# Kernel tuning notes

Measured on AMD Instinct MI355X. Metric: run time of the kernel, lower is better.

Reference implementation:

```python
import jax, jax.numpy as jnp
import numpy as np
from functools import partial

VS, VT, E, H = 32000, 32000, 512, 1024
B, S, T = 32, 64, 64


def gru_cell(x, h, Wih, Whh, bih, bhh):
    # PyTorch GRU gate order: r, z, n
    gi = x @ Wih.T + bih
    gh = h @ Whh.T + bhh
    ir, iz, inn = jnp.split(gi, 3, axis=-1)
    hr, hz, hn = jnp.split(gh, 3, axis=-1)
    r = jax.nn.sigmoid(ir + hr)
    z = jax.nn.sigmoid(iz + hz)
    n = jnp.tanh(inn + r * hn)
    return (1.0 - z) * n + z * h


def setup_inputs() -> dict:
    key = jax.random.key(0)
    ks = jax.random.split(key, 20)
    s = 0.02
    src = jax.random.randint(ks[0], (B, S), 0, VS)
    tgt = jax.random.randint(ks[1], (B, T), 0, VT)
    src_embed = (jax.random.normal(ks[2], (VS, E)) * s).at[0].set(0.0)  # padding_idx=0
    tgt_embed = (jax.random.normal(ks[3], (VT, E)) * s).at[0].set(0.0)
    enc_Wih = jax.random.normal(ks[4], (3 * H, E)) * s
    enc_Whh = jax.random.normal(ks[5], (3 * H, H)) * s
    enc_bih = jax.random.normal(ks[6], (3 * H,)) * s
    enc_bhh = jax.random.normal(ks[7], (3 * H,)) * s
    dec_Wih = jax.random.normal(ks[8], (3 * H, E + H)) * s
    dec_Whh = jax.random.normal(ks[9], (3 * H, H)) * s
    dec_bih = jax.random.normal(ks[10], (3 * H,)) * s
    dec_bhh = jax.random.normal(ks[11], (3 * H,)) * s
    attn_W = jax.random.normal(ks[12], (E, 2 * H)) * s
    attn_b = jax.random.normal(ks[13], (E,)) * s
    v_w = jax.random.normal(ks[14], (E,)) * s
    fc_W = jax.random.normal(ks[15], (VT, H)) * s
    fc_b = jax.random.normal(ks[16], (VT,)) * s
    return dict(src=src, tgt=tgt, src_embed=src_embed, tgt_embed=tgt_embed,
                enc_Wih=enc_Wih, enc_Whh=enc_Whh, enc_bih=enc_bih, enc_bhh=enc_bhh,
                dec_Wih=dec_Wih, dec_Whh=dec_Whh, dec_bih=dec_bih, dec_bhh=dec_bhh,
                attn_W=attn_W, attn_b=attn_b, v_w=v_w, fc_W=fc_W, fc_b=fc_b)


def reference(src, tgt, src_embed, tgt_embed, enc_Wih, enc_Whh, enc_bih, enc_bhh,
              dec_Wih, dec_Whh, dec_bih, dec_bhh, attn_W, attn_b, v_w, fc_W, fc_b):
    # --- encoder: GRU over src ---
    src_emb = src_embed[src]                      # [B,S,E]
    h0 = jnp.zeros((src.shape[0], H), src_emb.dtype)

    def enc_step(h, x):
        h2 = gru_cell(x, h, enc_Wih, enc_Whh, enc_bih, enc_bhh)
        return h2, h2

    h_last, enc_seq = jax.lax.scan(enc_step, h0, jnp.swapaxes(src_emb, 0, 1))
    enc = jnp.swapaxes(enc_seq, 0, 1)             # [B,S,H] encoder_outputs

    # attn linear splits: cat([hidden, enc]) @ attn_W.T == h@Wh.T + enc@We.T
    Wh, We = attn_W[:, :H], attn_W[:, H:]
    enc_proj = jnp.einsum('bsh,eh->bse', enc, We) + attn_b  # [B,S,E]

    # --- decoder with teacher forcing ratio = 1.0 (deterministic) ---
    def dec_step(h, tok):
        emb = tgt_embed[tok]                              # [B,E]
        energy = jnp.tanh(enc_proj + (h @ Wh.T)[:, None, :])  # [B,S,E]
        scores = jnp.einsum('bse,e->bs', energy, v_w)
        w = jax.nn.softmax(scores, axis=1)                # [B,S]
        ctx = jnp.einsum('bs,bsh->bh', w, enc)            # [B,H]
        x = jnp.concatenate([emb, ctx], axis=-1)          # [B,E+H]
        h2 = gru_cell(x, h, dec_Wih, dec_Whh, dec_bih, dec_bhh)
        logits = h2 @ fc_W.T + fc_b                       # [B,VT]
        return h2, logits

    _, logits = jax.lax.scan(dec_step, h_last, tgt[:, :-1].T)  # [T-1,B,VT]
    return jnp.swapaxes(logits, 0, 1)                     # [B,T-1,VT]
```

## Files before the change

kernel.cpp:

```cpp
#include <hip/hip_runtime.h>
#include <hip/hip_bf16.h>

typedef __hip_bfloat16 bf16;
typedef __attribute__((ext_vector_type(8))) __bf16 bf16x8;
typedef __attribute__((ext_vector_type(4))) float f32x4;
typedef __attribute__((ext_vector_type(4))) unsigned int u32x4;

#define DEVI __device__ __forceinline__

DEVI float sigm(float x) { return 1.f / (1.f + __expf(-x)); }
DEVI float tanh_fast(float x) { float e = __expf(2.f * x); return 1.f - 2.f / (e + 1.f); }
DEVI float lo2f(unsigned u) { return __uint_as_float(u << 16); }
DEVI float hi2f(unsigned u) { return __uint_as_float(u & 0xffff0000u); }

DEVI __bf16 f2b(float f) {
    unsigned u = __float_as_uint(f);
    u = u + 0x7FFFu + ((u >> 16) & 1u);
    unsigned short s = (unsigned short)(u >> 16);
    __bf16 b;
    __builtin_memcpy(&b, &s, 2);
    return b;
}
DEVI unsigned short b2u(__bf16 b) { unsigned short s; __builtin_memcpy(&s, &b, 2); return s; }

DEVI f32x4 MFMA(bf16x8 a, bf16x8 b, f32x4 c) {
    return __builtin_amdgcn_mfma_f32_16x16x32_bf16(a, b, c, 0, 0, 0);
}

DEVI bf16x8 load8(const bf16* p) { return *reinterpret_cast<const bf16x8*>(p); }
DEVI bf16x8 load8(const float* p) {
    float4 a = *reinterpret_cast<const float4*>(p);
    float4 b = *reinterpret_cast<const float4*>(p + 4);
    bf16x8 r;
    r[0] = f2b(a.x); r[1] = f2b(a.y); r[2] = f2b(a.z); r[3] = f2b(a.w);
    r[4] = f2b(b.x); r[5] = f2b(b.y); r[6] = f2b(b.z); r[7] = f2b(b.w);
    return r;
}

DEVI void storeOut(float* p, float v) { *p = v; }
DEVI void storeOut(bf16* p, float v) { *p = __float2bfloat16(v); }

#define WAIT_COHERENT() do { \
    asm volatile("s_waitcnt vmcnt(0)" ::: "memory"); \
    __builtin_amdgcn_sched_barrier(0); } while (0)

DEVI bf16x8 ld_cv16(const bf16* p) {
    u32x4 r;
    asm volatile("global_load_dwordx4 %0, %1, off sc0 sc1"
                 : "=v"(r) : "v"(p) : "memory");
    bf16x8 out;
    __builtin_memcpy(&out, &r, 16);
    return out;
}
DEVI f32x4 ld_cv16f(const float* p) {
    f32x4 r;
    asm volatile("global_load_dwordx4 %0, %1, off sc0 sc1"
                 : "=v"(r) : "v"(p) : "memory");
    return r;
}
DEVI unsigned ld_c_u32(const void* p) {
    unsigned r;
    asm volatile("global_load_dword %0, %1, off sc0 sc1"
                 : "=v"(r) : "v"(p) : "memory");
    return r;
}
DEVI void st_c_u32(void* p, unsigned v) {
    asm volatile("global_store_dword %0, %1, off sc0 sc1"
                 :: "v"(p), "v"(v) : "memory");
}

DEVI void gsync(unsigned* bar, unsigned target) {
    asm volatile("s_waitcnt vmcnt(0)" ::: "memory");
    __syncthreads();
    if (threadIdx.x == 0) {
        __hip_atomic_fetch_add(bar, 1u, __ATOMIC_RELAXED, __HIP_MEMORY_SCOPE_AGENT);
        while (atomicAdd(bar, 0u) < target) __builtin_amdgcn_s_sleep(8);
    }
    asm volatile("" ::: "memory");
    __syncthreads();
}

template<typename AT, typename BT, typename OT, bool GATHER, bool HASB>
__global__ __launch_bounds__(256)
void gemm_bt(const AT* __restrict__ A, const int* __restrict__ Aidx, int lda,
             const BT* __restrict__ B, int ldb, int boff,
             const float* __restrict__ bias,
             OT* __restrict__ C, long crs, long ccs,
             int M_real, int K)
{
    __shared__ __attribute__((aligned(16))) bf16 As[128 * 32];
    __shared__ __attribute__((aligned(16))) bf16 Bs[128 * 32];
    const int tid = threadIdx.x;
    const int lane = tid & 63;
    const int w = tid >> 6;
    const int wr = w >> 1, wc = w & 1;
    const int bm = blockIdx.y * 128;
    const int bn = blockIdx.x * 128;

    const int l16_0 = (2 * w + 0) * 64 + lane;
    const int l16_1 = (2 * w + 1) * 64 + lane;
    const int row0 = l16_0 >> 2, c0 = l16_0 & 3;
    const int row1 = l16_1 >> 2, c1 = l16_1 & 3;

    long arow0 = GATHER ? (long)Aidx[bm + row0] : (long)(bm + row0);
    long arow1 = GATHER ? (long)Aidx[bm + row1] : (long)(bm + row1);
    const AT* agp0 = A + arow0 * lda + c0 * 8;
    const AT* agp1 = A + arow1 * lda + c1 * 8;
    const BT* bgp0 = B + (long)(bn + row0) * ldb + boff + c0 * 8;
    const BT* bgp1 = B + (long)(bn + row1) * ldb + boff + c1 * 8;

    f32x4 acc[4][4];
    #pragma unroll
    for (int i = 0; i < 4; i++)
        #pragma unroll
        for (int j = 0; j < 4; j++) acc[i][j] = f32x4{0.f, 0.f, 0.f, 0.f};

    const bf16x8* Asv = reinterpret_cast<const bf16x8*>(As);
    const bf16x8* Bsv = reinterpret_cast<const bf16x8*>(Bs);
    bf16x8* AsW = reinterpret_cast<bf16x8*>(As);
    bf16x8* BsW = reinterpret_cast<bf16x8*>(Bs);
    const int kq = lane >> 4;
    const int lrow = lane & 15;

    bf16x8 ra0 = load8(agp0);
    bf16x8 ra1 = load8(agp1);
    bf16x8 rb0 = load8(bgp0);
    bf16x8 rb1 = load8(bgp1);

    for (int k0 = 0; k0 < K; k0 += 32) {
        __syncthreads();
        AsW[l16_0] = ra0; AsW[l16_1] = ra1;
        BsW[l16_0] = rb0; BsW[l16_1] = rb1;
        __syncthreads();

        const int kn = k0 + 32;
        if (kn < K) {
            ra0 = load8(agp0 + kn);
            ra1 = load8(agp1 + kn);
            rb0 = load8(bgp0 + kn);
            rb1 = load8(bgp1 + kn);
        }

        bf16x8 af[4], bfr[4];
        #pragma unroll
        for (int mt = 0; mt < 4; mt++) af[mt] = Asv[(wr * 64 + mt * 16 + lrow) * 4 + kq];
        #pragma unroll
        for (int nt = 0; nt < 4; nt++) bfr[nt] = Bsv[(wc * 64 + nt * 16 + lrow) * 4 + kq];
        #pragma unroll
        for (int mt = 0; mt < 4; mt++)
            #pragma unroll
            for (int nt = 0; nt < 4; nt++)
                acc[mt][nt] = MFMA(af[mt], bfr[nt], acc[mt][nt]);
    }

    const int rbase = kq * 4;
    #pragma unroll
    for (int nt = 0; nt < 4; nt++) {
        const int col = bn + wc * 64 + nt * 16 + lrow;
        float bv = 0.f;
        if (HASB) bv = bias[col];
        #pragma unroll
        for (int mt = 0; mt < 4; mt++) {
            const int rw = bm + wr * 64 + mt * 16 + rbase;
            #pragma unroll
            for (int r = 0; r < 4; r++) {
                const int row = rw + r;
                if (row < M_real) storeOut(&C[(long)row * crs + (long)col * ccs], acc[mt][nt][r] + bv);
            }
        }
    }
}

__global__ __launch_bounds__(256)
void gemm_fc(const bf16* __restrict__ A, const bf16* __restrict__ B,
             const float* __restrict__ bias, float* __restrict__ C)
{
    __shared__ __attribute__((aligned(16))) bf16 As[8192];
    __shared__ __attribute__((aligned(16))) bf16 Bs[8192];
    const int tid = threadIdx.x;
    const int bid = blockIdx.x;
    const int xcd = bid & 7;
    const int ii = bid >> 3;
    const int p = xcd + 8 * (ii >> 4);
    const int m = ii & 15;
    if (p >= 250) return;
    const int bm = m * 128, bn = p * 128;

    const int lane = tid & 63, w = tid >> 6, wr = w >> 1, wc = w & 1;
    const int kq = lane >> 4, lrow = lane & 15;

    int rowc[4], c8c[4];
    const bf16* gA[4];
    const bf16* gB[4];
    #pragma unroll
    for (int c = 0; c < 4; c++) {
        int q = c * 256 + tid;
        rowc[c] = q >> 3; c8c[c] = q & 7;
        gA[c] = A + (long)(bm + rowc[c]) * 1024 + c8c[c] * 8;
        gB[c] = B + (long)(bn + rowc[c]) * 1024 + c8c[c] * 8;
    }

    f32x4 acc[4][4];
    #pragma unroll
    for (int i = 0; i < 4; i++)
        #pragma unroll
        for (int j = 0; j < 4; j++) acc[i][j] = f32x4{0.f, 0.f, 0.f, 0.f};

    bf16x8* AsW = reinterpret_cast<bf16x8*>(As);
    bf16x8* BsW = reinterpret_cast<bf16x8*>(Bs);
    const bf16x8* Asv = reinterpret_cast<const bf16x8*>(As);
    const bf16x8* Bsv = reinterpret_cast<const bf16x8*>(Bs);

    bf16x8 ra[4], rb[4];
    #pragma unroll
    for (int c = 0; c < 4; c++) { ra[c] = load8(gA[c]); rb[c] = load8(gB[c]); }

    for (int kt = 0; kt < 16; ++kt) {
        __syncthreads();
        #pragma unroll
        for (int c = 0; c < 4; c++) {
            AsW[c8c[c] * 128 + rowc[c]] = ra[c];
            BsW[c8c[c] * 128 + rowc[c]] = rb[c];
        }
        __syncthreads();
        if (kt < 15) {
            const int ko = (kt + 1) * 64;
            #pragma unroll
            for (int c = 0; c < 4; c++) { ra[c] = load8(gA[c] + ko); rb[c] = load8(gB[c] + ko); }
        }
        #pragma unroll
        for (int h = 0; h < 2; ++h) {
            bf16x8 af[4], bfr[4];
            #pragma unroll
            for (int mt = 0; mt < 4; mt++) af[mt] = Asv[(h * 4 + kq) * 128 + wr * 64 + mt * 16 + lrow];
            #pragma unroll
            for (int nt = 0; nt < 4; nt++) bfr[nt] = Bsv[(h * 4 + kq) * 128 + wc * 64 + nt * 16 + lrow];
            #pragma unroll
            for (int mt = 0; mt < 4; mt++)
                #pragma unroll
                for (int nt = 0; nt < 4; nt++)
                    acc[mt][nt] = MFMA(af[mt], bfr[nt], acc[mt][nt]);
        }
    }

    const int rbase = kq * 4;
    #pragma unroll
    for (int nt = 0; nt < 4; nt++) {
        const int col = bn + wc * 64 + nt * 16 + lrow;
        const float bv = bias[col];
        #pragma unroll
        for (int mt = 0; mt < 4; mt++) {
            const int rw = bm + wr * 64 + mt * 16 + rbase;
            #pragma unroll
            for (int r = 0; r < 4; r++) {
                const int row = rw + r;
                if (row < 2016) C[(long)row * 32000 + col] = acc[mt][nt][r] + bv;
            }
        }
    }
}

__global__ __launch_bounds__(256)
void cvt_f32_bf16(const float* __restrict__ in, bf16* __restrict__ out, int n)
{
    int i = (blockIdx.x * blockDim.x + threadIdx.x) * 4;
    if (i < n) {
        float4 v = *reinterpret_cast<const float4*>(in + i);
        ushort4 o;
        o.x = b2u(f2b(v.x)); o.y = b2u(f2b(v.y));
        o.z = b2u(f2b(v.z)); o.w = b2u(f2b(v.w));
        *reinterpret_cast<ushort4*>(out + i) = o;
    }
}

__global__ __launch_bounds__(256)
void cvt_wh(const float* __restrict__ in, bf16* __restrict__ out)
{
    int i = (blockIdx.x * blockDim.x + threadIdx.x) * 4;
    if (i < 524288) {
        int e = i >> 10, k = i & 1023;
        float4 v = *reinterpret_cast<const float4*>(in + (size_t)e * 2048 + k);
        ushort4 o;
        o.x = b2u(f2b(v.x)); o.y = b2u(f2b(v.y));
        o.z = b2u(f2b(v.z)); o.w = b2u(f2b(v.w));
        *reinterpret_cast<ushort4*>(out + i) = o;
    }
}

__global__ __launch_bounds__(512, 1)
void enc_persist(bf16* __restrict__ h_bf,
                 const float* __restrict__ X,
                 const bf16* __restrict__ Whh, const float* __restrict__ bhh,
                 bf16* __restrict__ enc_out,
                 unsigned* __restrict__ bar)
{
    __shared__ float part[8][3][32][33];
    const int tid = threadIdx.x;
    const int lane = tid & 63;
    const int kw = tid >> 6;
    const int lrow = lane & 15;
    const int kq = lane >> 4;
    const int j0 = blockIdx.x * 32;

    const bf16x8* wv = reinterpret_cast<const bf16x8*>(Whh);
    bf16x8 wB[3][2][4];
    #pragma unroll
    for (int g = 0; g < 3; g++)
        #pragma unroll
        for (int jt = 0; jt < 2; jt++)
            #pragma unroll
            for (int kk = 0; kk < 4; kk++)
                wB[g][jt][kk] = wv[(size_t)(g * 1024 + j0 + jt * 16 + lrow) * 128 + kw * 16 + kq + kk * 4];

    const int bb = tid >> 4;
    const int jp = tid & 15;
    float bh[3][2];
    #pragma unroll
    for (int g = 0; g < 3; g++) {
        bh[g][0] = bhh[g * 1024 + j0 + jp * 2];
        bh[g][1] = bhh[g * 1024 + j0 + jp * 2 + 1];
    }
    float hprev[2] = {0.f, 0.f};
    unsigned sn = 0;

    for (int t = 0; t < 64; ++t) {
        const int cur = t & 1;
        const bf16* hbuf = h_bf + cur * 32768;

        bf16x8 af[2][4];
        #pragma unroll
        for (int bt = 0; bt < 2; bt++)
            #pragma unroll
            for (int kk = 0; kk < 4; kk++)
                af[bt][kk] = ld_cv16(hbuf + ((size_t)(bt * 16 + lrow) * 128 + kw * 16 + kq + kk * 4) * 8);

        const size_t xb = ((size_t)bb * 64 + t) * 3072 + j0 + jp * 2;
        float2 xg0 = *reinterpret_cast<const float2*>(X + xb);
        float2 xg1 = *reinterpret_cast<const float2*>(X + xb + 1024);
        float2 xg2 = *reinterpret_cast<const float2*>(X + xb + 2048);
        WAIT_COHERENT();

        f32x4 acc[3][2][2];
        #pragma unroll
        for (int g = 0; g < 3; g++)
            #pragma unroll
            for (int jt = 0; jt < 2; jt++)
                #pragma unroll
                for (int bt = 0; bt < 2; bt++) acc[g][jt][bt] = f32x4{0, 0, 0, 0};
        #pragma unroll
        for (int kk = 0; kk < 4; kk++)
            #pragma unroll
            for (int g = 0; g < 3; g++)
                #pragma unroll
                for (int jt = 0; jt < 2; jt++) {
                    acc[g][jt][0] = MFMA(af[0][kk], wB[g][jt][kk], acc[g][jt][0]);
                    acc[g][jt][1] = MFMA(af[1][kk], wB[g][jt][kk], acc[g][jt][1]);
                }
        #pragma unroll
        for (int g = 0; g < 3; g++)
            #pragma unroll
            for (int jt = 0; jt < 2; jt++)
                #pragma unroll
                for (int bt = 0; bt < 2; bt++)
                    #pragma unroll
                    for (int r = 0; r < 4; r++)
                        part[kw][g][bt * 16 + kq * 4 + r][jt * 16 + lrow] = acc[g][jt][bt][r];
        __syncthreads();

        float h2o[2];
        #pragma unroll
        for (int o = 0; o < 2; ++o) {
            const int jc = jp * 2 + o;
            float s0 = 0.f, s1 = 0.f, s2 = 0.f;
            #pragma unroll
            for (int ww = 0; ww < 8; ww++) {
                s0 += part[ww][0][bb][jc];
                s1 += part[ww][1][bb][jc];
                s2 += part[ww][2][bb][jc];
            }
            float x0 = o ? xg0.y : xg0.x;
            float x1 = o ? xg1.y : xg1.x;
            float x2 = o ? xg2.y : xg2.x;
            float rr = sigm(x0 + s0 + bh[0][o]);
            float zz = sigm(x1 + s1 + bh[1][o]);
            float nn = tanh_fast(x2 + rr * (s2 + bh[2][o]));
            h2o[o] = (1.f - zz) * nn + zz * hprev[o];
            hprev[o] = h2o[o];
        }
        unsigned pk = (unsigned)b2u(f2b(h2o[0])) | ((unsigned)b2u(f2b(h2o[1])) << 16);
        st_c_u32(h_bf + (cur ^ 1) * 32768 + bb * 1024 + j0 + jp * 2, pk);
        *reinterpret_cast<unsigned*>(enc_out + ((size_t)bb * 64 + t) * 1024 + j0 + jp * 2) = pk;

        if (t < 63) gsync(bar, ++sn * 32);
    }
}

__global__ __launch_bounds__(512, 1)
void dec_persist(bf16* __restrict__ h_bf,
                 const float* __restrict__ X,
                 const bf16* __restrict__ Whh, const float* __restrict__ bhh,
                 const bf16* __restrict__ encT0,
                 const bf16* __restrict__ encT1,
                 const bf16* __restrict__ encT2,
                 bf16* __restrict__ Hall,
                 const bf16* __restrict__ Wh_bf,
                 const bf16* __restrict__ enc_pj,
                 const float* __restrict__ v_w,
                 float* __restrict__ a_g,
                 float* __restrict__ w_g,
                 unsigned* __restrict__ bar)
{
    __shared__ float part[8][3][32][33];
    __shared__ float apart[8][16][32];
    __shared__ __attribute__((aligned(16))) float a_ls[512];
    __shared__ __attribute__((aligned(16))) float w_s[2048];
    __shared__ float sc_s[64];

    const int tid = threadIdx.x;
    const int lane = tid & 63;
    const int kw = tid >> 6;
    const int lrow = lane & 15;
    const int kq = lane >> 4;
    const int j0 = blockIdx.x * 32;
    const int e0 = blockIdx.x * 16;
    const int b = blockIdx.x;

    const bf16x8* wv = reinterpret_cast<const bf16x8*>(Whh);
    bf16x8 wB[3][2][4];
    #pragma unroll
    for (int g = 0; g < 3; g++)
        #pragma unroll
        for (int jt = 0; jt < 2; jt++)
            #pragma unroll
            for (int kk = 0; kk < 4; kk++)
                wB[g][jt][kk] = wv[(size_t)(g * 1024 + j0 + jt * 16 + lrow) * 128 + kw * 16 + kq + kk * 4];

    const bf16x8* whv = reinterpret_cast<const bf16x8*>(Wh_bf);
    bf16x8 whA[4];
    #pragma unroll
    for (int kk = 0; kk < 4; kk++)
        whA[kk] = whv[(size_t)(e0 + lrow) * 128 + kw * 16 + kq + kk * 4];

    float vr[8];
    #pragma unroll
    for (int ii = 0; ii < 8; ii++) vr[ii] = v_w[lane * 8 + ii];

    const int bb = tid >> 4;
    const int jp = tid & 15;
    float bh[3][2];
    #pragma unroll
    for (int g = 0; g < 3; g++) {
        bh[g][0] = bhh[g * 1024 + j0 + jp * 2];
        bh[g][1] = bhh[g * 1024 + j0 + jp * 2 + 1];
    }

    float hprev[2];
    {
        unsigned pk0 = ld_c_u32(h_bf + bb * 1024 + j0 + jp * 2);
        WAIT_COHERENT();
        hprev[0] = lo2f(pk0);
        hprev[1] = hi2f(pk0);
    }
    unsigned sn = 0;
    const bf16* encT[3] = {encT0, encT1, encT2};

    for (int t = 0; t < 63; ++t) {
        const int cur = t & 1;
        const bf16* hbuf = h_bf + cur * 32768;

        bf16x8 af[2][4];
        #pragma unroll
        for (int bt = 0; bt < 2; bt++)
            #pragma unroll
            for (int kk = 0; kk < 4; kk++)
                af[bt][kk] = ld_cv16(hbuf + ((size_t)(bt * 16 + lrow) * 128 + kw * 16 + kq + kk * 4) * 8);
        WAIT_COHERENT();

        {
            f32x4 aa[2] = {f32x4{0,0,0,0}, f32x4{0,0,0,0}};
            #pragma unroll
            for (int kk = 0; kk < 4; kk++) {
                aa[0] = MFMA(whA[kk], af[0][kk], aa[0]);
                aa[1] = MFMA(whA[kk], af[1][kk], aa[1]);
            }
            #pragma unroll
            for (int bt = 0; bt < 2; bt++)
                #pragma unroll
                for (int r = 0; r < 4; r++)
                    apart[kw][kq * 4 + r][bt * 16 + lrow] = aa[bt][r];
        }
        __syncthreads();
        {
            const int e = tid >> 5, bq = tid & 31;
            float s = 0.f;
            #pragma unroll
            for (int ww = 0; ww < 8; ww++) s += apart[ww][e][bq];
            st_c_u32(a_g + (size_t)(e0 + e) * 32 + bq, __float_as_uint(s));
        }
        gsync(bar, ++sn * 32);

        {
            unsigned av = ld_c_u32(a_g + (size_t)tid * 32 + b);
            WAIT_COHERENT();
            a_ls[tid] = __uint_as_float(av);
        }
        __syncthreads();
        #pragma unroll
        for (int si = 0; si < 8; ++si) {
            const int s = kw * 8 + si;
            u32x4 u = *reinterpret_cast<const u32x4*>(enc_pj + ((size_t)b * 64 + s) * 512 + lane * 8);
            float p = 0.f;
            #pragma unroll
            for (int i = 0; i < 4; ++i) {
                p += vr[2 * i]     * tanh_fast(lo2f(u[i]) + a_ls[lane * 8 + 2 * i]);
                p += vr[2 * i + 1] * tanh_fast(hi2f(u[i]) + a_ls[lane * 8 + 2 * i + 1]);
            }
            #pragma unroll
            for (int off = 32; off; off >>= 1) p += __shfl_xor(p, off);
            if (lane == 0) sc_s[s] = p;
        }
        __syncthreads();
        if (tid < 64) {
            float v = sc_s[tid], m = v;
            #pragma unroll
            for (int off = 32; off; off >>= 1) m = fmaxf(m, __shfl_xor(m, off));
            float e = __expf(v - m);
            float su = e;
            #pragma unroll
            for (int off = 32; off; off >>= 1) su += __shfl_xor(su, off);
            st_c_u32(w_g + b * 64 + tid, __float_as_uint(e / su));
        }
        gsync(bar, ++sn * 32);

        f32x4 wld = ld_cv16f(w_g + tid * 4);
        const size_t xb = ((size_t)bb * 63 + t) * 3072 + j0 + jp * 2;
        float2 xg0 = *reinterpret_cast<const float2*>(X + xb);
        float2 xg1 = *reinterpret_cast<const float2*>(X + xb + 1024);
        float2 xg2 = *reinterpret_cast<const float2*>(X + xb + 2048);
        WAIT_COHERENT();
        *reinterpret_cast<f32x4*>(&w_s[tid * 4]) = wld;

        f32x4 acc[3][2][2];
        #pragma unroll
        for (int g = 0; g < 3; g++)
            #pragma unroll
            for (int jt = 0; jt < 2; jt++)
                #pragma unroll
                for (int bt = 0; bt < 2; bt++) acc[g][jt][bt] = f32x4{0, 0, 0, 0};
        #pragma unroll
        for (int kk = 0; kk < 4; kk++)
            #pragma unroll
            for (int g = 0; g < 3; g++)
                #pragma unroll
                for (int jt = 0; jt < 2; jt++) {
                    acc[g][jt][0] = MFMA(af[0][kk], wB[g][jt][kk], acc[g][jt][0]);
                    acc[g][jt][1] = MFMA(af[1][kk], wB[g][jt][kk], acc[g][jt][1]);
                }
        #pragma unroll
        for (int g = 0; g < 3; g++)
            #pragma unroll
            for (int jt = 0; jt < 2; jt++)
                #pragma unroll
                for (int bt = 0; bt < 2; bt++)
                    #pragma unroll
                    for (int r = 0; r < 4; r++)
                        part[kw][g][bt * 16 + kq * 4 + r][jt * 16 + lrow] = acc[g][jt][bt][r];
        __syncthreads();

        float c0[3] = {0, 0, 0}, c1[3] = {0, 0, 0};
        #pragma unroll
        for (int g = 0; g < 3; g++) {
            const bf16* base = encT[g] + (size_t)bb * 64 * 1024 + j0 + jp * 2;
            #pragma unroll 8
            for (int s = 0; s < 64; ++s) {
                unsigned u = *reinterpret_cast<const unsigned*>(base + (size_t)s * 1024);
                float w = w_s[bb * 64 + s];
                c0[g] += lo2f(u) * w;
                c1[g] += hi2f(u) * w;
            }
        }

        float h2o[2];
        #pragma unroll
        for (int o = 0; o < 2; ++o) {
            const int jc = jp * 2 + o;
            float g0 = 0.f, g1 = 0.f, g2 = 0.f;
            #pragma unroll
            for (int ww = 0; ww < 8; ww++) {
                g0 += part[ww][0][bb][jc];
                g1 += part[ww][1][bb][jc];
                g2 += part[ww][2][bb][jc];
            }
            float cc0 = o ? c1[0] : c0[0];
            float cc1 = o ? c1[1] : c0[1];
            float cc2 = o ? c1[2] : c0[2];
            float x0 = o ? xg0.y : xg0.x;
            float x1 = o ? xg1.y : xg1.x;
            float x2 = o ? xg2.y : xg2.x;
            float rr = sigm(x0 + cc0 + g0 + bh[0][o]);
            float zz = sigm(x1 + cc1 + g1 + bh[1][o]);
            float nn = tanh_fast(x2 + cc2 + rr * (g2 + bh[2][o]));
            h2o[o] = (1.f - zz) * nn + zz * hprev[o];
            hprev[o] = h2o[o];
        }
        unsigned pk = (unsigned)b2u(f2b(h2o[0])) | ((unsigned)b2u(f2b(h2o[1])) << 16);
        st_c_u32(h_bf + (cur ^ 1) * 32768 + bb * 1024 + j0 + jp * 2, pk);
        *reinterpret_cast<unsigned*>(Hall + ((size_t)bb * 63 + t) * 1024 + j0 + jp * 2) = pk;

        if (t < 62) gsync(bar, ++sn * 32);
    }
}

__global__ void init_k(bf16* __restrict__ h0, bf16* __restrict__ hall_pad,
                       int* __restrict__ idx_dec,
                       const int* __restrict__ tgt, unsigned* __restrict__ bar)
{
    const int i = blockIdx.x * blockDim.x + threadIdx.x;
    if (i < 64) bar[i] = 0u;
    if (i < 32768) {
        h0[i] = __float2bfloat16(0.f);
        hall_pad[i] = __float2bfloat16(0.f);
    }
    if (i < 2048) {
        int v = 0;
        if (i < 2016) { int bq = i / 63; int tq = i - bq * 63; v = tgt[bq * 64 + tq]; }
        idx_dec[i] = v;
    }
}

extern "C" void kernel_launch(void* const* d_in, const int* in_sizes, int n_in,
                              void* d_out, int out_size, void* d_ws, size_t ws_size,
                              hipStream_t stream)
{
    const int*   src       = (const int*)d_in[0];
    const int*   tgt       = (const int*)d_in[1];
    const float* src_embed = (const float*)d_in[2];
    const float* tgt_embed = (const float*)d_in[3];
    const float* enc_Wih   = (const float*)d_in[4];
    const float* enc_Whh   = (const float*)d_in[5];
    const float* enc_bih   = (const float*)d_in[6];
    const float* enc_bhh   = (const float*)d_in[7];
    const float* dec_Wih   = (const float*)d_in[8];
    const float* dec_Whh   = (const float*)d_in[9];
    const float* dec_bih   = (const float*)d_in[10];
    const float* dec_bhh   = (const float*)d_in[11];
    const float* attn_W    = (const float*)d_in[12];
    const float* attn_b    = (const float*)d_in[13];
    const float* v_w       = (const float*)d_in[14];
    const float* fc_W      = (const float*)d_in[15];
    const float* fc_b      = (const float*)d_in[16];

    char* w = (char*)d_ws;
    unsigned* bar      = (unsigned*)(w);
    float* X_enc       = (float*)(w + 256);
    float* X_dec       = (float*)(w + 25166080);
    bf16*  enc_bf      = (bf16*) (w + 50331904);
    bf16*  enc_pj_bf   = (bf16*) (w + 54526208);
    bf16*  H_all       = (bf16*) (w + 56623360);
    bf16*  h_bf        = (bf16*) (w + 60817664);
    float* w_g         = (float*)(w + 60948736);
    float* a_g         = (float*)(w + 60956928);
    int*   idx_dec     = (int*)  (w + 61022464);
    bf16*  enc_Whh_bf  = (bf16*) (w + 61030656);
    bf16*  dec_Whh_bf  = (bf16*) (w + 67322112);
    bf16*  Wh_bf       = (bf16*) (w + 73613568);
    bf16*  encT0       = (bf16*) (w + 74662144);
    bf16*  encT1       = (bf16*) (w + 78856448);
    bf16*  encT2       = (bf16*) (w + 83050752);
    bf16*  fc_W_bf     = (bf16*) (w + 87245056);

    init_k<<<128, 256, 0, stream>>>(h_bf, H_all + 2016 * 1024, idx_dec, tgt, bar);
    cvt_f32_bf16<<<3072, 256, 0, stream>>>(enc_Whh, enc_Whh_bf, 3145728);
    cvt_f32_bf16<<<3072, 256, 0, stream>>>(dec_Whh, dec_Whh_bf, 3145728);
    cvt_f32_bf16<<<32000, 256, 0, stream>>>(fc_W, fc_W_bf, 32768000);
    cvt_wh<<<512, 256, 0, stream>>>(attn_W, Wh_bf);

    gemm_bt<float, float, float, true, true><<<dim3(24, 16), 256, 0, stream>>>(
        src_embed, src, 512, enc_Wih, 512, 0, enc_bih, X_enc, 3072, 1, 2048, 512);
    gemm_bt<float, float, float, true, true><<<dim3(24, 16), 256, 0, stream>>>(
        tgt_embed, idx_dec, 512, dec_Wih, 1536, 0, dec_bih, X_dec, 3072, 1, 2048, 512);

    enc_persist<<<32, 512, 0, stream>>>(h_bf, X_enc, enc_Whh_bf, enc_bhh, enc_bf, bar);

    gemm_bt<bf16, float, bf16, false, true><<<dim3(4, 16), 256, 0, stream>>>(
        enc_bf, nullptr, 1024, attn_W, 2048, 1024, attn_b, enc_pj_bf, 512, 1, 2048, 1024);

    gemm_bt<bf16, float, bf16, false, false><<<dim3(8, 16), 256, 0, stream>>>(
        enc_bf, nullptr, 1024, dec_Wih + (size_t)0 * 1024 * 1536, 1536, 512, nullptr, encT0, 1024, 1, 2048, 1024);
    gemm_bt<bf16, float, bf16, false, false><<<dim3(8, 16), 256, 0, stream>>>(
        enc_bf, nullptr, 1024, dec_Wih + (size_t)1 * 1024 * 1536, 1536, 512, nullptr, encT1, 1024, 1, 2048, 1024);
    gemm_bt<bf16, float, bf16, false, false><<<dim3(8, 16), 256, 0, stream>>>(
        enc_bf, nullptr, 1024, dec_Wih + (size_t)2 * 1024 * 1536, 1536, 512, nullptr, encT2, 1024, 1, 2048, 1024);

    dec_persist<<<32, 512, 0, stream>>>(h_bf, X_dec, dec_Whh_bf, dec_bhh,
                                        encT0, encT1, encT2,
                                        H_all, Wh_bf, enc_pj_bf, v_w,
                                        a_g, w_g, bar + 32);

    gemm_fc<<<4096, 256, 0, stream>>>(H_all, fc_W_bf, fc_b, (float*)d_out);
}
```

Before: 3.076 ms.

## Compute attention hidden projection redundantly per block to drop a grid barrier

Each decoder block now computes the full h@Wh^T projection for its own batch row. It reads a repacked bf16 Wh from global memory with a scalar FMA loop, replacing the distributed MFMA computation that was exchanged through global memory and a grid-wide barrier. This removes one global sync and its round trip through memory per decoder step, at the cost of every block streaming the whole 1 MB Wh each step. The barrier spin sleep is also shortened to cut wake-up latency.

Measured after the change: 6.182 ms. 101% more time.

```diff
diff --git a/kernel.cpp b/kernel.cpp
--- a/kernel.cpp
+++ b/kernel.cpp
@@ -74,7 +74,7 @@
     __syncthreads();
     if (threadIdx.x == 0) {
         __hip_atomic_fetch_add(bar, 1u, __ATOMIC_RELAXED, __HIP_MEMORY_SCOPE_AGENT);
-        while (atomicAdd(bar, 0u) < target) __builtin_amdgcn_s_sleep(8);
+        while (atomicAdd(bar, 0u) < target) __builtin_amdgcn_s_sleep(1);
     }
     asm volatile("" ::: "memory");
     __syncthreads();
@@ -274,16 +274,23 @@
 }
 
 __global__ __launch_bounds__(256)
-void cvt_wh(const float* __restrict__ in, bf16* __restrict__ out)
-{
-    int i = (blockIdx.x * blockDim.x + threadIdx.x) * 4;
-    if (i < 524288) {
-        int e = i >> 10, k = i & 1023;
-        float4 v = *reinterpret_cast<const float4*>(in + (size_t)e * 2048 + k);
-        ushort4 o;
-        o.x = b2u(f2b(v.x)); o.y = b2u(f2b(v.y));
-        o.z = b2u(f2b(v.z)); o.w = b2u(f2b(v.w));
-        *reinterpret_cast<ushort4*>(out + i) = o;
+void cvt_whp(const float* __restrict__ in, bf16* __restrict__ out)
+{
+    int t = blockIdx.x * blockDim.x + threadIdx.x;
+    if (t < 65536) {
+        const int e = t >> 7;
+        const int k8 = t & 127;
+        const float* src = in + (size_t)e * 2048 + k8 * 8;
+        float4 a = *reinterpret_cast<const float4*>(src);
+        float4 b = *reinterpret_cast<const float4*>(src + 4);
+        ushort4 o0, o1;
+        o0.x = b2u(f2b(a.x)); o0.y = b2u(f2b(a.y));
+        o0.z = b2u(f2b(a.z)); o0.w = b2u(f2b(a.w));
+        o1.x = b2u(f2b(b.x)); o1.y = b2u(f2b(b.y));
+        o1.z = b2u(f2b(b.z)); o1.w = b2u(f2b(b.w));
+        bf16* dst = out + ((size_t)k8 * 512 + e) * 8;
+        *reinterpret_cast<ushort4*>(dst) = o0;
+        *reinterpret_cast<ushort4*>(dst + 4) = o1;
     }
 }
 
@@ -403,15 +410,14 @@
                  const bf16* __restrict__ encT1,
                  const bf16* __restrict__ encT2,
                  bf16* __restrict__ Hall,
-                 const bf16* __restrict__ Wh_bf,
+                 const bf16* __restrict__ Whp,
                  const bf16* __restrict__ enc_pj,
                  const float* __restrict__ v_w,
-                 float* __restrict__ a_g,
                  float* __restrict__ w_g,
                  unsigned* __restrict__ bar)
 {
     __shared__ float part[8][3][32][33];
-    __shared__ float apart[8][16][32];
+    __shared__ __attribute__((aligned(16))) float hbl[1024];
     __shared__ __attribute__((aligned(16))) float a_ls[512];
     __shared__ __attribute__((aligned(16))) float w_s[2048];
     __shared__ float sc_s[64];
@@ -422,7 +428,6 @@
     const int lrow = lane & 15;
     const int kq = lane >> 4;
     const int j0 = blockIdx.x * 32;
-    const int e0 = blockIdx.x * 16;
     const int b = blockIdx.x;
 
     const bf16x8* wv = reinterpret_cast<const bf16x8*>(Whh);
@@ -434,12 +439,6 @@
             #pragma unroll
             for (int kk = 0; kk < 4; kk++)
                 wB[g][jt][kk] = wv[(size_t)(g * 1024 + j0 + jt * 16 + lrow) * 128 + kw * 16 + kq + kk * 4];
-
-    const bf16x8* whv = reinterpret_cast<const bf16x8*>(Wh_bf);
-    bf16x8 whA[4];
-    #pragma unroll
-    for (int kk = 0; kk < 4; kk++)
-        whA[kk] = whv[(size_t)(e0 + lrow) * 128 + kw * 16 + kq + kk * 4];
 
     float vr[8];
     #pragma unroll
@@ -474,37 +473,29 @@
             #pragma unroll
             for (int kk = 0; kk < 4; kk++)
                 af[bt][kk] = ld_cv16(hbuf + ((size_t)(bt * 16 + lrow) * 128 + kw * 16 + kq + kk * 4) * 8);
+        unsigned uh = ld_c_u32(hbuf + b * 1024 + tid * 2);
         WAIT_COHERENT();
+        hbl[tid * 2]     = lo2f(uh);
+        hbl[tid * 2 + 1] = hi2f(uh);
+        __syncthreads();
 
         {
-            f32x4 aa[2] = {f32x4{0,0,0,0}, f32x4{0,0,0,0}};
-            #pragma unroll
-            for (int kk = 0; kk < 4; kk++) {
-                aa[0] = MFMA(whA[kk], af[0][kk], aa[0]);
-                aa[1] = MFMA(whA[kk], af[1][kk], aa[1]);
+            const u32x4* wp = reinterpret_cast<const u32x4*>(Whp);
+            float s = 0.f;
+            #pragma unroll 4
+            for (int k8 = 0; k8 < 128; ++k8) {
+                u32x4 u = wp[k8 * 512 + tid];
+                const float* hp = &hbl[k8 * 8];
+                #pragma unroll
+                for (int i = 0; i < 4; ++i) {
+                    s += lo2f(u[i]) * hp[2 * i];
+                    s += hi2f(u[i]) * hp[2 * i + 1];
+                }
             }
-            #pragma unroll
-            for (int bt = 0; bt < 2; bt++)
-                #pragma unroll
-                for (int r = 0; r < 4; r++)
-                    apart[kw][kq * 4 + r][bt * 16 + lrow] = aa[bt][r];
-        }
-        __syncthreads();
-        {
-            const int e = tid >> 5, bq = tid & 31;
-            float s = 0.f;
-            #pragma unroll
-            for (int ww = 0; ww < 8; ww++) s += apart[ww][e][bq];
-            st_c_u32(a_g + (size_t)(e0 + e) * 32 + bq, __float_as_uint(s));
-        }
-        gsync(bar, ++sn * 32);
-
-        {
-            unsigned av = ld_c_u32(a_g + (size_t)tid * 32 + b);
-            WAIT_COHERENT();
-            a_ls[tid] = __uint_as_float(av);
-        }
-        __syncthreads();
+            a_ls[tid] = s;
+        }
+        __syncthreads();
+
         #pragma unroll
         for (int si = 0; si < 8; ++si) {
             const int s = kw * 8 + si;
@@ -659,11 +650,10 @@
     bf16*  H_all       = (bf16*) (w + 56623360);
     bf16*  h_bf        = (bf16*) (w + 60817664);
     float* w_g         = (float*)(w + 60948736);
-    float* a_g         = (float*)(w + 60956928);
     int*   idx_dec     = (int*)  (w + 61022464);
     bf16*  enc_Whh_bf  = (bf16*) (w + 61030656);
     bf16*  dec_Whh_bf  = (bf16*) (w + 67322112);
-    bf16*  Wh_bf       = (bf16*) (w + 73613568);
+    bf16*  Whp         = (bf16*) (w + 73613568);
     bf16*  encT0       = (bf16*) (w + 74662144);
     bf16*  encT1       = (bf16*) (w + 78856448);
     bf16*  encT2       = (bf16*) (w + 83050752);
@@ -673,7 +663,7 @@
     cvt_f32_bf16<<<3072, 256, 0, stream>>>(enc_Whh, enc_Whh_bf, 3145728);
     cvt_f32_bf16<<<3072, 256, 0, stream>>>(dec_Whh, dec_Whh_bf, 3145728);
     cvt_f32_bf16<<<32000, 256, 0, stream>>>(fc_W, fc_W_bf, 32768000);
-    cvt_wh<<<512, 256, 0, stream>>>(attn_W, Wh_bf);
+    cvt_whp<<<256, 256, 0, stream>>>(attn_W, Whp);
 
     gemm_bt<float, float, float, true, true><<<dim3(24, 16), 256, 0, stream>>>(
         src_embed, src, 512, enc_Wih, 512, 0, enc_bih, X_enc, 3072, 1, 2048, 512);
@@ -694,8 +684,8 @@
 
     dec_persist<<<32, 512, 0, stream>>>(h_bf, X_dec, dec_Whh_bf, dec_bhh,
                                         encT0, encT1, encT2,
-                                        H_all, Wh_bf, enc_pj_bf, v_w,
-                                        a_g, w_g, bar + 32);
+                                        H_all, Whp, enc_pj_bf, v_w,
+                                        w_g, bar + 32);
 
     gemm_fc<<<4096, 256, 0, stream>>>(H_all, fc_W_bf, fc_b, (float*)d_out);
 }
```
